# Performance work log

Measured on AMD Instinct MI355X. Metric: run time of the kernel, lower is better.

The kernel has to match this reference:

```python
import jax, jax.numpy as jnp
import numpy as np

B, T, P, D, S, R = 4, 128, 256, 512, 64, 8  # batch, window, patches, d_model, n_state, dt_rank


def setup_inputs() -> dict:
    key = jax.random.key(0)
    ks = jax.random.split(key, 8)
    sc = 0.02  # weight init scale
    return {
        "X": jax.random.normal(ks[0], (B, T, P, D), jnp.float32),
        "H0": jnp.zeros((B, P, S), jnp.float32),
        "a_hat": jax.random.normal(ks[1], (S,), jnp.float32),
        "U_w": jax.random.normal(ks[2], (S, D), jnp.float32) * sc,
        "sB_w": jax.random.normal(ks[3], (S, D), jnp.float32) * sc,
        "sB_b": jnp.zeros((S,), jnp.float32),
        "sC_w": jax.random.normal(ks[4], (S, D), jnp.float32) * sc,
        "sC_b": jnp.zeros((S,), jnp.float32),
        "sD1_w": jax.random.normal(ks[5], (R, D), jnp.float32) * sc,
        "sD1_b": jnp.zeros((R,), jnp.float32),
        "sD2_w": jax.random.normal(ks[6], (1, R), jnp.float32) * sc,
        "sD2_b": jnp.zeros((1,), jnp.float32),
        "ro_w": jax.random.normal(ks[7], (D, S), jnp.float32) * sc,
    }


def reference(X, H0, a_hat, U_w, sB_w, sB_b, sC_w, sC_b, sD1_w, sD1_b, sD2_w, sD2_b, ro_w):
    eps = 1e-12
    logA = -jnp.exp(a_hat)                                    # [S]
    # selective (input-dependent) parameters
    u = jnp.einsum('btpd,sd->btps', X, U_w)                   # [B,T,P,S]
    B_t = jnp.einsum('btpd,sd->btps', X, sB_w) + sB_b
    C_t = jnp.einsum('btpd,sd->btps', X, sC_w) + sC_b
    dt_feat = jax.nn.silu(jnp.einsum('btpd,rd->btpr', X, sD1_w) + sD1_b)
    dt = jax.nn.softplus(jnp.einsum('btpr,or->btpo', dt_feat, sD2_w) + sD2_b)  # [B,T,P,1]
    A = jnp.exp(dt * logA)                                    # [B,T,P,S] via broadcast
    b = (1.0 - A) * (B_t * u)
    # prefix-product scan: h_t = A_t*h_{t-1} + b_t  ->  h_t = P_t*(H0 + cumsum(b/P))
    Pc = jnp.cumprod(jnp.maximum(A, eps), axis=1)             # [B,T,P,S]
    invP = 1.0 / jnp.maximum(Pc, eps)
    c = jnp.cumsum(b * invP, axis=1)
    H_seq = Pc * (H0[:, None] + c)                            # [B,T,P,S]
    Y_seq = jnp.einsum('btps,ds->btpd', C_t * H_seq, ro_w)    # [B,T,P,D]
    Y_seq = Y_seq.reshape(X.shape[0], -1, X.shape[-1])        # [B, T*P, D]
    H_T = H_seq[:, -1]                                        # [B,P,S]
    return (H_seq, Y_seq, H_T)
```

## Files before the change

kernel.cpp:

```cpp
#include <hip/hip_runtime.h>
#include <hip/hip_bf16.h>
#include <math.h>

namespace {
constexpr int B_N = 4, T_N = 128, P_N = 256, D_N = 512, S_N = 64;
constexpr int NTH = 512;
constexpr int KC  = 32;
constexpr int NCH = D_N / KC;

constexpr int XS0_OFF = 0;
constexpr int WS0_OFF = 8192;
constexpr int XS1_OFF = 24576;
constexpr int WS1_OFF = 32768;
constexpr int BU_OFF  = 0;
constexpr int CH_OFF  = 16384;
constexpr int ROS0_OFF= 32768;
constexpr int ROS1_OFF= 0;
constexpr int DT_OFF  = 49152;
constexpr int LDS_BYTES = 49664;

constexpr int WIMG_ELEMS  = NCH * 256 * 32;
constexpr int ROIMG_ELEMS = 4 * 128 * 64;
}

typedef short bf16x8 __attribute__((ext_vector_type(8)));
typedef float f32x4  __attribute__((ext_vector_type(4)));

__device__ __forceinline__ unsigned short f2b(float f) {
    unsigned int x = __float_as_uint(f);
    return (unsigned short)((x + 0x7FFFu + ((x >> 16) & 1u)) >> 16);
}
__device__ __forceinline__ float b2f(unsigned short h) {
    return __uint_as_float(((unsigned int)h) << 16);
}
__device__ __forceinline__ unsigned int pk2(float lo, float hi) {
    union { __hip_bfloat162 h; unsigned int u; } cv;
    cv.h = __float22bfloat162_rn(float2{lo, hi});
    return cv.u;
}
__device__ __forceinline__ int swz32(int row, int col) {
    return row * 32 + (col ^ (((row >> 1) & 3) << 3));
}
__device__ __forceinline__ int swz64(int row, int col) {
    return row * 64 + (col ^ ((row & 7) << 3));
}
__device__ __forceinline__ void cvtstore8(unsigned short* dst, float4 a, float4 b) {
    uint4 r;
    r.x = pk2(a.x, a.y); r.y = pk2(a.z, a.w);
    r.z = pk2(b.x, b.y); r.w = pk2(b.z, b.w);
    *(uint4*)dst = r;
}

__global__ __launch_bounds__(512) void mamba_prep(
    const float* __restrict__ U_w, const float* __restrict__ sB_w,
    const float* __restrict__ sC_w, const float* __restrict__ sD1_w,
    const float* __restrict__ ro_w,
    unsigned short* __restrict__ wImg, unsigned short* __restrict__ roImg)
{
    const int idx = blockIdx.x * 512 + threadIdx.x;
    if (idx < WIMG_ELEMS) {
        const int kc = idx >> 13, rem = idx & 8191, r = rem >> 5, c = rem & 31;
        float v = 0.0f;
        if (r < 192) {
            const int g = r >> 4, w = r & 15, tr = g % 3, sb = g / 3;
            const float* base = (tr == 0) ? U_w : (tr == 1) ? sB_w : sC_w;
            v = base[(size_t)(sb * 16 + w) * D_N + kc * KC + c];
        } else if (r < 200) {
            v = sD1_w[(size_t)(r - 192) * D_N + kc * KC + c];
        }
        wImg[kc * 8192 + swz32(r, c)] = f2b(v);
    } else if (idx < WIMG_ELEMS + ROIMG_ELEMS) {
        const int j = idx - WIMG_ELEMS;
        const int pp = j >> 13, rem = j & 8191, r = rem >> 6, c = rem & 63;
        roImg[pp * 8192 + swz64(r, c)] = f2b(ro_w[(size_t)(pp * 128 + r) * S_N + c]);
    }
}

__global__ __launch_bounds__(NTH, 4) void mamba_mfma(
    const float* __restrict__ X, const float* __restrict__ H0,
    const float* __restrict__ a_hat,
    const float* __restrict__ sB_b, const float* __restrict__ sC_b,
    const float* __restrict__ sD1_b, const float* __restrict__ sD2_w,
    const float* __restrict__ sD2_b,
    const unsigned short* __restrict__ wImg, const unsigned short* __restrict__ roImg,
    float* __restrict__ Hseq, float* __restrict__ Y, float* __restrict__ HT)
{
    __shared__ __align__(16) char smem[LDS_BYTES];
    float* DTB = (float*)(smem + DT_OFF);

    const int tid  = threadIdx.x;
    const int lane = tid & 63;
    const int wid  = tid >> 6;
    const int wm   = wid >> 2;
    const int wn   = wid & 3;
    const int l15  = lane & 15;
    const int lg   = lane >> 4;
    const int b    = blockIdx.x >> 8;
    const int p    = blockIdx.x & 255;

    const float la  = (tid < 64) ? -expf(a_hat[tid]) : 0.0f;
    const float h0v = (tid < 64) ? H0[((size_t)b * P_N + p) * S_N + tid] : 0.0f;

    f32x4 acc[4][3];
    f32x4 accdt;
    #pragma unroll
    for (int q = 0; q < 4; ++q) accdt[q] = 0.0f;
    #pragma unroll
    for (int mf = 0; mf < 4; ++mf)
        #pragma unroll
        for (int nf = 0; nf < 3; ++nf)
            #pragma unroll
            for (int q = 0; q < 4; ++q) acc[mf][nf][q] = 0.0f;

    const int xr = tid >> 2, xq = tid & 3;
    const float* xsrc = X + (((size_t)b * T_N + xr) * P_N + p) * D_N + xq * 8;
    const int xoff = swz32(xr, xq * 8);

    const char* wImgB = (const char*)wImg;

    float4 xA = *(const float4*)(xsrc), xB = *(const float4*)(xsrc + 4);
    uint4 wpA = *((const uint4*)(wImgB) + tid * 2);
    uint4 wpB = *((const uint4*)(wImgB) + tid * 2 + 1);
    cvtstore8((unsigned short*)(smem + XS0_OFF) + xoff, xA, xB);
    *((uint4*)(smem + WS0_OFF) + tid * 2)     = wpA;
    *((uint4*)(smem + WS0_OFF) + tid * 2 + 1) = wpB;
    {
        const float* nx = xsrc + KC;
        xA = *(const float4*)(nx); xB = *(const float4*)(nx + 4);
        wpA = *((const uint4*)(wImgB + 16384) + tid * 2);
        wpB = *((const uint4*)(wImgB + 16384) + tid * 2 + 1);
    }
    __syncthreads();

    const int kb = lg * 8;
    #pragma unroll 2
    for (int kc = 0; kc < NCH; ++kc) {
        unsigned short* XSc = (unsigned short*)(smem + ((kc & 1) ? XS1_OFF : XS0_OFF));
        unsigned short* WSc = (unsigned short*)(smem + ((kc & 1) ? WS1_OFF : WS0_OFF));
        char*           XSn = smem + ((kc & 1) ? XS0_OFF : XS1_OFF);
        char*           WSn = smem + ((kc & 1) ? WS0_OFF : WS1_OFF);
        if (kc + 1 < NCH) {
            cvtstore8((unsigned short*)XSn + xoff, xA, xB);
            *((uint4*)WSn + tid * 2)     = wpA;
            *((uint4*)WSn + tid * 2 + 1) = wpB;
        }
        if (kc + 2 < NCH) {
            const float* nx = xsrc + (kc + 2) * KC;
            xA = *(const float4*)(nx); xB = *(const float4*)(nx + 4);
            wpA = *((const uint4*)(wImgB + (kc + 2) * 16384) + tid * 2);
            wpB = *((const uint4*)(wImgB + (kc + 2) * 16384) + tid * 2 + 1);
        }
        __builtin_amdgcn_s_setprio(1);
        bf16x8 a[4];
        #pragma unroll
        for (int mf = 0; mf < 4; ++mf)
            a[mf] = *(const bf16x8*)&XSc[swz32(wm * 64 + mf * 16 + l15, kb)];
        #pragma unroll
        for (int nf = 0; nf < 3; ++nf) {
            bf16x8 bb = *(const bf16x8*)&WSc[swz32(wn * 48 + nf * 16 + l15, kb)];
            #pragma unroll
            for (int mf = 0; mf < 4; ++mf)
                acc[mf][nf] = __builtin_amdgcn_mfma_f32_16x16x32_bf16(a[mf], bb, acc[mf][nf], 0, 0, 0);
        }
        {
            bf16x8 adt = *(const bf16x8*)&XSc[swz32(wid * 16 + l15, kb)];
            bf16x8 bd  = *(const bf16x8*)&WSc[swz32(192 + l15, kb)];
            accdt = __builtin_amdgcn_mfma_f32_16x16x32_bf16(adt, bd, accdt, 0, 0, 0);
        }
        __builtin_amdgcn_s_setprio(0);
        __syncthreads();
    }

    {
        unsigned short* BU  = (unsigned short*)(smem + BU_OFF);
        unsigned short* CHB = (unsigned short*)(smem + CH_OFF);
        const int s = wn * 16 + l15;
        const float biasB = sB_b[s], biasC = sC_b[s];
        #pragma unroll
        for (int mf = 0; mf < 4; ++mf) {
            #pragma unroll
            for (int q = 0; q < 4; ++q) {
                const int t = wm * 64 + mf * 16 + lg * 4 + q;
                const float u  = acc[mf][0][q];
                const float Bv = acc[mf][1][q] + biasB;
                const float Cv = acc[mf][2][q] + biasC;
                BU[t * 64 + s]   = f2b(Bv * u);
                CHB[swz64(t, s)] = f2b(Cv);
            }
        }
    }
    {
        const float w2 = (l15 < 8) ? sD2_w[l15] : 0.0f;
        const float b1 = (l15 < 8) ? sD1_b[l15] : 0.0f;
        const float b2 = sD2_b[0];
        #pragma unroll
        for (int q = 0; q < 4; ++q) {
            float z = accdt[q] + b1;
            float w = (z / (1.0f + expf(-z))) * w2;
            w = (l15 < 8) ? w : 0.0f;
            w += __shfl_xor(w, 1);
            w += __shfl_xor(w, 2);
            w += __shfl_xor(w, 4);
            if (l15 == 0) {
                float zz = w + b2;
                DTB[wid * 16 + lg * 4 + q] = (zz > 20.0f) ? zz : log1pf(expf(zz));
            }
        }
    }
    __syncthreads();

    if (tid < 64) {
        unsigned short* BU  = (unsigned short*)(smem + BU_OFF);
        unsigned short* CHB = (unsigned short*)(smem + CH_OFF);
        const int s = tid;
        float Pcv = 1.0f, cv = 0.0f, Hv = 0.0f;
        float* hout = Hseq + ((size_t)b * T_N * P_N + p) * S_N + s;
        for (int t = 0; t < T_N; ++t) {
            const float Av = expf(DTB[t] * la);
            const float bv = (1.0f - Av) * b2f(BU[t * 64 + s]);
            Pcv *= fmaxf(Av, 1e-12f);
            cv += bv * (1.0f / fmaxf(Pcv, 1e-12f));
            Hv = Pcv * (h0v + cv);
            hout[(size_t)t * P_N * S_N] = Hv;
            const int e = swz64(t, s);
            CHB[e] = f2b(b2f(CHB[e]) * Hv);
        }
        HT[((size_t)b * P_N + p) * S_N + s] = Hv;
    } else {
        for (int u = tid - 64; u < 512; u += 448) {
            uint4 a0 = *((const uint4*)roImg + u * 2);
            uint4 a1 = *((const uint4*)roImg + u * 2 + 1);
            *((uint4*)(smem + ROS0_OFF) + u * 2)     = a0;
            *((uint4*)(smem + ROS0_OFF) + u * 2 + 1) = a1;
        }
    }
    __syncthreads();

    bf16x8 af0[4], af1[4];
    {
        unsigned short* CHB = (unsigned short*)(smem + CH_OFF);
        #pragma unroll
        for (int mf = 0; mf < 4; ++mf) {
            af0[mf] = *(const bf16x8*)&CHB[swz64(wm * 64 + mf * 16 + l15, lg * 8)];
            af1[mf] = *(const bf16x8*)&CHB[swz64(wm * 64 + mf * 16 + l15, 32 + lg * 8)];
        }
    }

    for (int pp = 0; pp < 4; ++pp) {
        unsigned short* cur = (unsigned short*)(smem + ((pp & 1) ? ROS1_OFF : ROS0_OFF));
        char*           nxt = smem + ((pp & 1) ? ROS0_OFF : ROS1_OFF);
        uint4 npA, npB;
        if (pp < 3) {
            const uint4* s = (const uint4*)((const char*)roImg + (pp + 1) * 16384) + tid * 2;
            npA = s[0]; npB = s[1];
        }
        f32x4 yacc[4][2];
        #pragma unroll
        for (int mf = 0; mf < 4; ++mf)
            #pragma unroll
            for (int nf = 0; nf < 2; ++nf)
                #pragma unroll
                for (int q = 0; q < 4; ++q) yacc[mf][nf][q] = 0.0f;
        #pragma unroll
        for (int nf = 0; nf < 2; ++nf) {
            bf16x8 bb0 = *(const bf16x8*)&cur[swz64(wn * 32 + nf * 16 + l15, lg * 8)];
            bf16x8 bb1 = *(const bf16x8*)&cur[swz64(wn * 32 + nf * 16 + l15, 32 + lg * 8)];
            #pragma unroll
            for (int mf = 0; mf < 4; ++mf) {
                yacc[mf][nf] = __builtin_amdgcn_mfma_f32_16x16x32_bf16(af0[mf], bb0, yacc[mf][nf], 0, 0, 0);
                yacc[mf][nf] = __builtin_amdgcn_mfma_f32_16x16x32_bf16(af1[mf], bb1, yacc[mf][nf], 0, 0, 0);
            }
        }
        if (pp < 3) {
            *((uint4*)nxt + tid * 2)     = npA;
            *((uint4*)nxt + tid * 2 + 1) = npB;
        }
        #pragma unroll
        for (int mf = 0; mf < 4; ++mf) {
            const int t0 = wm * 64 + mf * 16 + lg * 4;
            float* ybase = Y + (((size_t)b * T_N + t0) * P_N + p) * D_N + pp * 128 + wn * 32 + l15;
            #pragma unroll
            for (int nf = 0; nf < 2; ++nf) {
                #pragma unroll
                for (int q = 0; q < 4; ++q)
                    ybase[(size_t)q * P_N * D_N + nf * 16] = yacc[mf][nf][q];
            }
        }
        if (pp < 3) __syncthreads();
    }
}

extern "C" void kernel_launch(void* const* d_in, const int* in_sizes, int n_in,
                              void* d_out, int out_size, void* d_ws, size_t ws_size,
                              hipStream_t stream) {
    const float* X     = (const float*)d_in[0];
    const float* H0    = (const float*)d_in[1];
    const float* a_hat = (const float*)d_in[2];
    const float* U_w   = (const float*)d_in[3];
    const float* sB_w  = (const float*)d_in[4];
    const float* sB_b  = (const float*)d_in[5];
    const float* sC_w  = (const float*)d_in[6];
    const float* sC_b  = (const float*)d_in[7];
    const float* sD1_w = (const float*)d_in[8];
    const float* sD1_b = (const float*)d_in[9];
    const float* sD2_w = (const float*)d_in[10];
    const float* sD2_b = (const float*)d_in[11];
    const float* ro_w  = (const float*)d_in[12];

    float* out   = (float*)d_out;
    float* HseqP = out;
    float* YP    = out + (size_t)B_N * T_N * P_N * S_N;
    float* HTP   = YP  + (size_t)B_N * T_N * P_N * D_N;

    unsigned short* wImg  = (unsigned short*)d_ws;
    unsigned short* roImg = (unsigned short*)((char*)d_ws + 262144);

    hipLaunchKernelGGL(mamba_prep, dim3((WIMG_ELEMS + ROIMG_ELEMS) / 512), dim3(512), 0, stream,
                       U_w, sB_w, sC_w, sD1_w, ro_w, wImg, roImg);
    hipLaunchKernelGGL(mamba_mfma, dim3(B_N * P_N), dim3(NTH), 0, stream,
                       X, H0, a_hat, sB_b, sC_b, sD1_b, sD2_w, sD2_b,
                       wImg, roImg, HseqP, YP, HTP);
}
```

Measured before the change: 153.7 us.

## Load weight tiles directly into LDS with global_load_lds and explicit vmcnt barriers

Weight chunks for the projection GEMM and the readout weights now go straight from global memory into LDS through the direct global-to-LDS load builtin. This bypasses the register staging and the separate LDS stores. The main loop is split so the first 13 chunks use a hand-written waitcnt/barrier macro with sched barriers, and X prefetch moves two chunks ahead using alternating even/odd register sets. This cuts VGPR use and instruction count, but it relies on exact vmcnt accounting for correctness and adds scheduling constraints.

```diff
diff --git a/kernel.cpp b/kernel.cpp
--- a/kernel.cpp
+++ b/kernel.cpp
@@ -50,6 +50,17 @@
     r.z = pk2(b.x, b.y); r.w = pk2(b.z, b.w);
     *(uint4*)dst = r;
 }
+__device__ __forceinline__ void gload16(const void* g, void* l) {
+    __builtin_amdgcn_global_load_lds(
+        (const __attribute__((address_space(1))) unsigned int*)g,
+        (__attribute__((address_space(3))) unsigned int*)l, 16, 0, 0);
+}
+#define CBAR(N) do { \
+    __builtin_amdgcn_sched_barrier(0); \
+    asm volatile("s_waitcnt vmcnt(" #N ") lgkmcnt(0)" ::: "memory"); \
+    __builtin_amdgcn_s_barrier(); \
+    __builtin_amdgcn_sched_barrier(0); \
+} while (0)
 
 __global__ __launch_bounds__(512) void mamba_prep(
     const float* __restrict__ U_w, const float* __restrict__ sB_w,
@@ -95,8 +106,11 @@
     const int wn   = wid & 3;
     const int l15  = lane & 15;
     const int lg   = lane >> 4;
+    const int lane16 = lane * 16;
     const int b    = blockIdx.x >> 8;
     const int p    = blockIdx.x & 255;
+    const char* wImgB  = (const char*)wImg;
+    const char* roImgB = (const char*)roImg;
 
     const float la  = (tid < 64) ? -expf(a_hat[tid]) : 0.0f;
     const float h0v = (tid < 64) ? H0[((size_t)b * P_N + p) * S_N + tid] : 0.0f;
@@ -116,39 +130,67 @@
     const float* xsrc = X + (((size_t)b * T_N + xr) * P_N + p) * D_N + xq * 8;
     const int xoff = swz32(xr, xq * 8);
 
-    const char* wImgB = (const char*)wImg;
-
-    float4 xA = *(const float4*)(xsrc), xB = *(const float4*)(xsrc + 4);
-    uint4 wpA = *((const uint4*)(wImgB) + tid * 2);
-    uint4 wpB = *((const uint4*)(wImgB) + tid * 2 + 1);
-    cvtstore8((unsigned short*)(smem + XS0_OFF) + xoff, xA, xB);
-    *((uint4*)(smem + WS0_OFF) + tid * 2)     = wpA;
-    *((uint4*)(smem + WS0_OFF) + tid * 2 + 1) = wpB;
+    float4 xe0, xe1, xo0, xo1;
     {
-        const float* nx = xsrc + KC;
-        xA = *(const float4*)(nx); xB = *(const float4*)(nx + 4);
-        wpA = *((const uint4*)(wImgB + 16384) + tid * 2);
-        wpB = *((const uint4*)(wImgB + 16384) + tid * 2 + 1);
-    }
-    __syncthreads();
+        float4 t0 = *(const float4*)(xsrc), t1 = *(const float4*)(xsrc + 4);
+        cvtstore8((unsigned short*)(smem + XS0_OFF) + xoff, t0, t1);
+        gload16(wImgB + wid * 2048 + lane16,        smem + WS0_OFF + wid * 2048);
+        gload16(wImgB + wid * 2048 + 1024 + lane16, smem + WS0_OFF + wid * 2048 + 1024);
+        __builtin_amdgcn_sched_barrier(0);
+        const float* n1 = xsrc + 1 * KC;
+        xo0 = *(const float4*)(n1); xo1 = *(const float4*)(n1 + 4);
+        const float* n2 = xsrc + 2 * KC;
+        xe0 = *(const float4*)(n2); xe1 = *(const float4*)(n2 + 4);
+    }
+    CBAR(4);
 
     const int kb = lg * 8;
     #pragma unroll 2
-    for (int kc = 0; kc < NCH; ++kc) {
+    for (int kc = 0; kc < 13; ++kc) {
+        unsigned short* XSc = (unsigned short*)(smem + ((kc & 1) ? XS1_OFF : XS0_OFF));
+        unsigned short* WSc = (unsigned short*)(smem + ((kc & 1) ? WS1_OFF : WS0_OFF));
+        char*           XSn = smem + ((kc & 1) ? XS0_OFF : XS1_OFF);
+        char*           WSn = smem + ((kc & 1) ? WS0_OFF : WS1_OFF);
+        if ((kc + 1) & 1) cvtstore8((unsigned short*)XSn + xoff, xo0, xo1);
+        else              cvtstore8((unsigned short*)XSn + xoff, xe0, xe1);
+        gload16(wImgB + (kc + 1) * 16384 + wid * 2048 + lane16,        WSn + wid * 2048);
+        gload16(wImgB + (kc + 1) * 16384 + wid * 2048 + 1024 + lane16, WSn + wid * 2048 + 1024);
+        __builtin_amdgcn_sched_barrier(0);
+        {
+            const float* nx = xsrc + (kc + 3) * KC;
+            if ((kc + 1) & 1) { xo0 = *(const float4*)(nx); xo1 = *(const float4*)(nx + 4); }
+            else              { xe0 = *(const float4*)(nx); xe1 = *(const float4*)(nx + 4); }
+        }
+        __builtin_amdgcn_s_setprio(1);
+        bf16x8 a[4];
+        #pragma unroll
+        for (int mf = 0; mf < 4; ++mf)
+            a[mf] = *(const bf16x8*)&XSc[swz32(wm * 64 + mf * 16 + l15, kb)];
+        #pragma unroll
+        for (int nf = 0; nf < 3; ++nf) {
+            bf16x8 bb = *(const bf16x8*)&WSc[swz32(wn * 48 + nf * 16 + l15, kb)];
+            #pragma unroll
+            for (int mf = 0; mf < 4; ++mf)
+                acc[mf][nf] = __builtin_amdgcn_mfma_f32_16x16x32_bf16(a[mf], bb, acc[mf][nf], 0, 0, 0);
+        }
+        {
+            bf16x8 adt = *(const bf16x8*)&XSc[swz32(wid * 16 + l15, kb)];
+            bf16x8 bd  = *(const bf16x8*)&WSc[swz32(192 + l15, kb)];
+            accdt = __builtin_amdgcn_mfma_f32_16x16x32_bf16(adt, bd, accdt, 0, 0, 0);
+        }
+        __builtin_amdgcn_s_setprio(0);
+        CBAR(2);
+    }
+    for (int kc = 13; kc < NCH; ++kc) {
         unsigned short* XSc = (unsigned short*)(smem + ((kc & 1) ? XS1_OFF : XS0_OFF));
         unsigned short* WSc = (unsigned short*)(smem + ((kc & 1) ? WS1_OFF : WS0_OFF));
         char*           XSn = smem + ((kc & 1) ? XS0_OFF : XS1_OFF);
         char*           WSn = smem + ((kc & 1) ? WS0_OFF : WS1_OFF);
         if (kc + 1 < NCH) {
-            cvtstore8((unsigned short*)XSn + xoff, xA, xB);
-            *((uint4*)WSn + tid * 2)     = wpA;
-            *((uint4*)WSn + tid * 2 + 1) = wpB;
-        }
-        if (kc + 2 < NCH) {
-            const float* nx = xsrc + (kc + 2) * KC;
-            xA = *(const float4*)(nx); xB = *(const float4*)(nx + 4);
-            wpA = *((const uint4*)(wImgB + (kc + 2) * 16384) + tid * 2);
-            wpB = *((const uint4*)(wImgB + (kc + 2) * 16384) + tid * 2 + 1);
+            if ((kc + 1) & 1) cvtstore8((unsigned short*)XSn + xoff, xo0, xo1);
+            else              cvtstore8((unsigned short*)XSn + xoff, xe0, xe1);
+            gload16(wImgB + (kc + 1) * 16384 + wid * 2048 + lane16,        WSn + wid * 2048);
+            gload16(wImgB + (kc + 1) * 16384 + wid * 2048 + 1024 + lane16, WSn + wid * 2048 + 1024);
         }
         __builtin_amdgcn_s_setprio(1);
         bf16x8 a[4];
@@ -227,12 +269,8 @@
         }
         HT[((size_t)b * P_N + p) * S_N + s] = Hv;
     } else {
-        for (int u = tid - 64; u < 512; u += 448) {
-            uint4 a0 = *((const uint4*)roImg + u * 2);
-            uint4 a1 = *((const uint4*)roImg + u * 2 + 1);
-            *((uint4*)(smem + ROS0_OFF) + u * 2)     = a0;
-            *((uint4*)(smem + ROS0_OFF) + u * 2 + 1) = a1;
-        }
+        for (int seg = wid - 1; seg < 16; seg += 7)
+            gload16(roImgB + seg * 1024 + lane16, smem + ROS0_OFF + seg * 1024);
     }
     __syncthreads();
 
@@ -249,10 +287,9 @@
     for (int pp = 0; pp < 4; ++pp) {
         unsigned short* cur = (unsigned short*)(smem + ((pp & 1) ? ROS1_OFF : ROS0_OFF));
         char*           nxt = smem + ((pp & 1) ? ROS0_OFF : ROS1_OFF);
-        uint4 npA, npB;
         if (pp < 3) {
-            const uint4* s = (const uint4*)((const char*)roImg + (pp + 1) * 16384) + tid * 2;
-            npA = s[0]; npB = s[1];
+            gload16(roImgB + (pp + 1) * 16384 + wid * 2048 + lane16,        nxt + wid * 2048);
+            gload16(roImgB + (pp + 1) * 16384 + wid * 2048 + 1024 + lane16, nxt + wid * 2048 + 1024);
         }
         f32x4 yacc[4][2];
         #pragma unroll
@@ -270,10 +307,6 @@
                 yacc[mf][nf] = __builtin_amdgcn_mfma_f32_16x16x32_bf16(af0[mf], bb0, yacc[mf][nf], 0, 0, 0);
                 yacc[mf][nf] = __builtin_amdgcn_mfma_f32_16x16x32_bf16(af1[mf], bb1, yacc[mf][nf], 0, 0, 0);
             }
-        }
-        if (pp < 3) {
-            *((uint4*)nxt + tid * 2)     = npA;
-            *((uint4*)nxt + tid * 2 + 1) = npB;
         }
         #pragma unroll
         for (int mf = 0; mf < 4; ++mf) {
```

After: 159.8 us. 3.9% more time.
